# Optimization experiments

Hardware: AMD Instinct MI355X
Metric: run time of the kernel (lower is better)

The kernel has to match this reference:

```python
import jax, jax.numpy as jnp
import numpy as np

DIM = 192
N_HEADS = 8
HEAD_DIM = DIM // N_HEADS
SCALE = 1.0 / np.sqrt(HEAD_DIM).astype(np.float32)
H_GRID, W_GRID = 32, 64
KH, KW = 7, 11


def build_local_mask():
    # Equivalent to the torch double-loop construction: token (h2,w2) may attend
    # to (h,w) iff |h2-h| <= KH//2 and |w2-w| <= KW//2 (odd kernels).
    hh = jnp.arange(H_GRID)
    ww = jnp.arange(W_GRID)
    dh_ok = jnp.abs(hh[:, None] - hh[None, :]) <= KH // 2  # [H, H]
    dw_ok = jnp.abs(ww[:, None] - ww[None, :]) <= KW // 2  # [W, W]
    allowed = dh_ok[:, None, :, None] & dw_ok[None, :, None, :]  # [H, W, H, W]
    allowed = allowed.reshape(H_GRID * W_GRID, H_GRID * W_GRID)
    return jnp.where(allowed, 0.0, -jnp.inf).astype(jnp.float32)  # [N, N]


def setup_inputs() -> dict:
    key = jax.random.key(0)
    ks = jax.random.split(key, 5)
    B, N = 4, H_GRID * W_GRID
    w_std = 1.0 / np.sqrt(DIM)
    x = jax.random.normal(ks[0], (B, N, DIM), dtype=jnp.float32)
    qkv_w = jax.random.normal(ks[1], (3 * DIM, DIM), dtype=jnp.float32) * w_std
    qkv_b = jax.random.normal(ks[2], (3 * DIM,), dtype=jnp.float32) * 0.02
    proj_w = jax.random.normal(ks[3], (DIM, DIM), dtype=jnp.float32) * w_std
    proj_b = jax.random.normal(ks[4], (DIM,), dtype=jnp.float32) * 0.02
    mask = build_local_mask()
    return {"x": x, "qkv_w": qkv_w, "qkv_b": qkv_b,
            "proj_w": proj_w, "proj_b": proj_b, "mask": mask}


def reference(x, qkv_w, qkv_b, proj_w, proj_b, mask):
    B, N, _ = x.shape
    qkv = x @ qkv_w.T + qkv_b                              # [B, N, 3*DIM]
    qkv = qkv.reshape(B, N, 3, N_HEADS, HEAD_DIM)
    qkv = jnp.transpose(qkv, (2, 0, 3, 1, 4))              # [3, B, h, N, d]
    q, k, v = qkv[0] * SCALE, qkv[1], qkv[2]
    attn = jnp.einsum('bhnd,bhmd->bhnm', q, k) + mask      # [B, h, N, N]
    attn = jax.nn.softmax(attn, axis=-1)                   # == log_softmax().exp()
    out = jnp.einsum('bhnm,bhmd->bhnd', attn, v)           # [B, h, N, d]
    out = jnp.transpose(out, (0, 2, 1, 3)).reshape(B, N, DIM)
    return out @ proj_w.T + proj_b
```

## Files before the change

kernel.cpp:

```cpp
#include <hip/hip_runtime.h>
#include <math.h>

#define H_GRID 32
#define W_GRID 64
#define NTOK   2048
#define NHEADS 8
#define HD     24
#define DIMC   192
#define BATCH  4

static constexpr float SCALE = 0.20412414523193154f;

typedef unsigned short ushort;
typedef unsigned int   uint;
typedef __attribute__((ext_vector_type(8))) short bf16x8;
typedef __attribute__((ext_vector_type(4))) float f32x4;

static __device__ __forceinline__ float4 ld4(const float* p) { return *(const float4*)p; }

static __device__ __forceinline__ ushort f2bf(float f) {
    union { float f; uint u; } c; c.f = f;
    uint u = c.u;
    uint r = u + 0x7fffu + ((u >> 16) & 1u);
    return (ushort)(r >> 16);
}
static __device__ __forceinline__ float bf2f(ushort h) {
    union { uint u; float f; } c; c.u = ((uint)h) << 16; return c.f;
}

__global__ __launch_bounds__(256) void cast_w(const float* __restrict__ wq,
                                              const float* __restrict__ wp,
                                              ushort* __restrict__ wqhi, ushort* __restrict__ wqlo,
                                              ushort* __restrict__ wphi, ushort* __restrict__ wplo) {
    const int i = blockIdx.x * 256 + threadIdx.x;
    const float* src; ushort *dh, *dl; int off;
    if (i < 27648) { src = wq; dh = wqhi; dl = wqlo; off = i; }
    else           { src = wp; dh = wphi; dl = wplo; off = i - 27648; }
    float4 v = ld4(src + (size_t)off * 4);
    float a[4] = {v.x, v.y, v.z, v.w};
    ushort h[4], l[4];
#pragma unroll
    for (int j = 0; j < 4; j++) {
        h[j] = f2bf(a[j]);
        l[j] = f2bf(a[j] - bf2f(h[j]));
    }
    *(ushort4*)(dh + (size_t)off * 4) = make_ushort4(h[0], h[1], h[2], h[3]);
    *(ushort4*)(dl + (size_t)off * 4) = make_ushort4(l[0], l[1], l[2], l[3]);
}

__global__ __launch_bounds__(256) void gemm_qkv(const float* __restrict__ A,
                                                const ushort* __restrict__ Wh,
                                                const ushort* __restrict__ Wl,
                                                const float* __restrict__ bias,
                                                float* __restrict__ C) {
    __shared__ ushort Wsh[64 * 200];
    __shared__ ushort Wsl[64 * 200];

    const int t    = threadIdx.x;
    const int wave = t >> 6, lane = t & 63;
    const int m0   = blockIdx.x * 64 + wave * 16;
    const int j0   = blockIdx.y * 64;
    const int row  = lane & 15;
    const int kq   = lane >> 4;

    for (int i = t; i < 1536; i += 256) {
        const int r = i / 24, c = i - (i / 24) * 24;
        *(uint4*)&Wsh[r * 200 + c * 8] = *(const uint4*)&Wh[(size_t)(j0 + r) * 192 + c * 8];
        *(uint4*)&Wsl[r * 200 + c * 8] = *(const uint4*)&Wl[(size_t)(j0 + r) * 192 + c * 8];
    }

    const float* pA = A + (size_t)(m0 + row) * 192 + kq * 8;

    f32x4 acc[4] = {f32x4{0,0,0,0}, f32x4{0,0,0,0}, f32x4{0,0,0,0}, f32x4{0,0,0,0}};

    __syncthreads();

#pragma unroll
    for (int ks = 0; ks < 6; ks++) {
        float4 a0 = ld4(pA + ks * 32);
        float4 a1 = ld4(pA + ks * 32 + 4);
        float av[8] = {a0.x, a0.y, a0.z, a0.w, a1.x, a1.y, a1.z, a1.w};
        bf16x8 afh, afl;
#pragma unroll
        for (int j = 0; j < 8; j++) {
            ushort hh = f2bf(av[j]);
            afh[j] = (short)hh;
            afl[j] = (short)f2bf(av[j] - bf2f(hh));
        }
#pragma unroll
        for (int nt = 0; nt < 4; nt++) {
            const int widx = (nt * 16 + row) * 200 + kq * 8 + ks * 32;
            bf16x8 bh = *(const bf16x8*)&Wsh[widx];
            bf16x8 bl = *(const bf16x8*)&Wsl[widx];
            acc[nt] = __builtin_amdgcn_mfma_f32_16x16x32_bf16(afh, bh, acc[nt], 0, 0, 0);
            acc[nt] = __builtin_amdgcn_mfma_f32_16x16x32_bf16(afl, bh, acc[nt], 0, 0, 0);
            acc[nt] = __builtin_amdgcn_mfma_f32_16x16x32_bf16(afh, bl, acc[nt], 0, 0, 0);
        }
    }

#pragma unroll
    for (int nt = 0; nt < 4; nt++) {
        const int col = j0 + nt * 16 + row;
        const float bv = bias[col];
#pragma unroll
        for (int r = 0; r < 4; r++) {
            const int m = m0 + kq * 4 + r;
            C[(size_t)m * 576 + col] = acc[nt][r] + bv;
        }
    }
}

__global__ __launch_bounds__(256) void attn_mfma(const float* __restrict__ qkv,
                                                 ushort* __restrict__ ahi,
                                                 ushort* __restrict__ alo) {
    const int qtile = blockIdx.x;
    const int head  = blockIdx.y;
    const int b     = blockIdx.z;
    const int qh0   = (qtile >> 3) * 4;
    const int qw0   = (qtile & 7) * 8;

    const int kh0 = max(qh0 - 3, 0), kh1 = min(qh0 + 6, H_GRID - 1);
    const int kw0 = max(qw0 - 5, 0), kw1 = min(qw0 + 12, W_GRID - 1);
    const int khc = kh1 - kh0 + 1;
    const int kwc = kw1 - kw0 + 1;
    const int nk  = khc * kwc;

    const int t = threadIdx.x;
    const int w = t >> 6, lane = t & 63;
    const int n16 = lane & 15, quad = lane >> 4;

    __shared__ __align__(16) char sm[67584];
    ushort* Khi   = (ushort*)(sm);
    ushort* Klo   = (ushort*)(sm + 15360);
    ushort* Phi   = (ushort*)(sm);
    ushort* Plo   = (ushort*)(sm + 14848);
    ushort* Qhi   = (ushort*)(sm + 30720);
    ushort* Qlo   = (ushort*)(sm + 33280);
    ushort* VThi  = (ushort*)(sm + 35840);
    ushort* VTlo  = (ushort*)(sm + 50688);
    int*    khw   = (int*)(sm + 65536);
    int*    toks  = (int*)(sm + 66304);
    float*  mxbuf = (float*)(sm + 67072);
    float*  sumbuf= (float*)(sm + 67328);

    const float* base = qkv + (size_t)(b * 2048) * 576 + head * 24;

    if (t < 192) {
        if (t < nk) {
            const int rr = t / kwc;
            const int cc = t - rr * kwc;
            khw[t]  = ((kh0 + rr) << 8) | (kw0 + cc);
            toks[t] = ((kh0 + rr) << 6) + (kw0 + cc);
        } else {
            khw[t] = 0x7F7F;
        }
    }
    __syncthreads();

    for (int i = t; i < 768; i += 256) {
        const int s = i >> 2, g = i & 3;
        ushort h[8], l[8];
        if (g < 3 && s < nk) {
            const float* src = base + (size_t)toks[s] * 576 + 192 + g * 8;
            float4 a = ld4(src), c = ld4(src + 4);
            float vs[8] = {a.x, a.y, a.z, a.w, c.x, c.y, c.z, c.w};
#pragma unroll
            for (int j = 0; j < 8; j++) { h[j] = f2bf(vs[j]); l[j] = f2bf(vs[j] - bf2f(h[j])); }
        } else {
#pragma unroll
            for (int j = 0; j < 8; j++) { h[j] = 0; l[j] = 0; }
        }
        *(uint4*)&Khi[s * 40 + g * 8] = *(uint4*)h;
        *(uint4*)&Klo[s * 40 + g * 8] = *(uint4*)l;
    }
    if (t < 128) {
        const int r = t >> 2, g = t & 3;
        ushort h[8], l[8];
        if (g < 3) {
            const int tq = ((qh0 + (r >> 3)) << 6) + qw0 + (r & 7);
            const float* src = base + (size_t)tq * 576 + g * 8;
            float4 a = ld4(src), c = ld4(src + 4);
            float vs[8] = {a.x * SCALE, a.y * SCALE, a.z * SCALE, a.w * SCALE,
                           c.x * SCALE, c.y * SCALE, c.z * SCALE, c.w * SCALE};
#pragma unroll
            for (int j = 0; j < 8; j++) { h[j] = f2bf(vs[j]); l[j] = f2bf(vs[j] - bf2f(h[j])); }
        } else {
#pragma unroll
            for (int j = 0; j < 8; j++) { h[j] = 0; l[j] = 0; }
        }
        *(uint4*)&Qhi[r * 40 + g * 8] = *(uint4*)h;
        *(uint4*)&Qlo[r * 40 + g * 8] = *(uint4*)l;
    }
    for (int i = t; i < 1152; i += 256) {
        const int dq = i / 192, s = i - (i / 192) * 192;
        float4 vv = make_float4(0.f, 0.f, 0.f, 0.f);
        if (s < nk) vv = ld4(base + (size_t)toks[s] * 576 + 384 + dq * 4);
        float vs[4] = {vv.x, vv.y, vv.z, vv.w};
#pragma unroll
        for (int c = 0; c < 4; c++) {
            const int d = dq * 4 + c;
            ushort hh = f2bf(vs[c]);
            VThi[d * 232 + s] = hh;
            VTlo[d * 232 + s] = f2bf(vs[c] - bf2f(hh));
        }
    }
    for (int j = t; j < 1536; j += 256) {
        const int d = 24 + j / 192, s = j - (j / 192) * 192;
        VThi[d * 232 + s] = 0;
        VTlo[d * 232 + s] = 0;
    }
    __syncthreads();

    const int mt = w >> 1, nth = w & 1;
    const bf16x8 qfh = *(const bf16x8*)&Qhi[(16 * mt + n16) * 40 + quad * 8];
    const bf16x8 qfl = *(const bf16x8*)&Qlo[(16 * mt + n16) * 40 + quad * 8];

    f32x4 sc[6];
    int khwv[6];
#pragma unroll
    for (int j = 0; j < 6; j++) {
        const int slot = (nth * 6 + j) * 16 + n16;
        const bf16x8 kfh = *(const bf16x8*)&Khi[slot * 40 + quad * 8];
        const bf16x8 kfl = *(const bf16x8*)&Klo[slot * 40 + quad * 8];
        f32x4 a = f32x4{0, 0, 0, 0};
        a = __builtin_amdgcn_mfma_f32_16x16x32_bf16(qfh, kfh, a, 0, 0, 0);
        a = __builtin_amdgcn_mfma_f32_16x16x32_bf16(qfl, kfh, a, 0, 0, 0);
        a = __builtin_amdgcn_mfma_f32_16x16x32_bf16(qfh, kfl, a, 0, 0, 0);
        sc[j] = a;
        khwv[j] = khw[slot];
    }

    const int m0r = quad * 4;
    float sv[6][4];
    float mx4[4] = {-1e30f, -1e30f, -1e30f, -1e30f};
#pragma unroll
    for (int j = 0; j < 6; j++) {
        const int kh = khwv[j] >> 8, kw = khwv[j] & 255;
#pragma unroll
        for (int r = 0; r < 4; r++) {
            const int m = 16 * mt + m0r + r;
            const bool valid = (abs(kh - (qh0 + (m >> 3))) <= 3) &&
                               (abs(kw - (qw0 + (m & 7))) <= 5);
            const float s = valid ? sc[j][r] : -1e30f;
            sv[j][r] = s;
            mx4[r] = fmaxf(mx4[r], s);
        }
    }
#pragma unroll
    for (int d = 1; d < 16; d <<= 1)
#pragma unroll
        for (int r = 0; r < 4; r++) mx4[r] = fmaxf(mx4[r], __shfl_xor(mx4[r], d));
    if (n16 == 0) {
#pragma unroll
        for (int r = 0; r < 4; r++) mxbuf[w * 16 + m0r + r] = mx4[r];
    }
    __syncthreads();
#pragma unroll
    for (int r = 0; r < 4; r++) mx4[r] = fmaxf(mx4[r], mxbuf[(w ^ 1) * 16 + m0r + r]);

    float sum4[4] = {0.f, 0.f, 0.f, 0.f};
#pragma unroll
    for (int j = 0; j < 6; j++) {
        const int col = (nth * 6 + j) * 16 + n16;
#pragma unroll
        for (int r = 0; r < 4; r++) {
            const float p = __expf(sv[j][r] - mx4[r]);
            sum4[r] += p;
            const int m = 16 * mt + m0r + r;
            const ushort ph = f2bf(p);
            Phi[m * 232 + col] = ph;
            Plo[m * 232 + col] = f2bf(p - bf2f(ph));
        }
    }
#pragma unroll
    for (int d = 1; d < 16; d <<= 1)
#pragma unroll
        for (int r = 0; r < 4; r++) sum4[r] += __shfl_xor(sum4[r], d);
    if (n16 == 0) {
#pragma unroll
        for (int r = 0; r < 4; r++) sumbuf[w * 16 + m0r + r] = sum4[r];
    }
    __syncthreads();

    const int mtP = w >> 1, ntP = w & 1;
    f32x4 accA = f32x4{0,0,0,0}, accB = f32x4{0,0,0,0}, accC = f32x4{0,0,0,0};
#pragma unroll
    for (int ks = 0; ks < 6; ks++) {
        const int ko = ks * 32 + quad * 8;
        const bf16x8 pa = *(const bf16x8*)&Phi[(16 * mtP + n16) * 232 + ko];
        const bf16x8 pl = *(const bf16x8*)&Plo[(16 * mtP + n16) * 232 + ko];
        const bf16x8 va = *(const bf16x8*)&VThi[(16 * ntP + n16) * 232 + ko];
        const bf16x8 vl = *(const bf16x8*)&VTlo[(16 * ntP + n16) * 232 + ko];
        accA = __builtin_amdgcn_mfma_f32_16x16x32_bf16(pa, va, accA, 0, 0, 0);
        accB = __builtin_amdgcn_mfma_f32_16x16x32_bf16(pl, va, accB, 0, 0, 0);
        accC = __builtin_amdgcn_mfma_f32_16x16x32_bf16(pa, vl, accC, 0, 0, 0);
    }

    const int d = 16 * ntP + n16;
    if (d < 24) {
#pragma unroll
        for (int r = 0; r < 4; r++) {
            const int m   = 16 * mtP + quad * 4 + r;
            const float tot = sumbuf[(2 * mtP) * 16 + (m & 15)] +
                              sumbuf[(2 * mtP + 1) * 16 + (m & 15)];
            const float val = (accA[r] + accB[r] + accC[r]) / tot;
            const int tq = ((qh0 + (m >> 3)) << 6) + qw0 + (m & 7);
            const size_t ob = (size_t)(b * 2048 + tq) * 192 + head * 24 + d;
            const ushort hh = f2bf(val);
            ahi[ob] = hh;
            alo[ob] = f2bf(val - bf2f(hh));
        }
    }
}

__global__ __launch_bounds__(128) void gemm_proj(const ushort* __restrict__ Ahi,
                                                 const ushort* __restrict__ Alo,
                                                 const ushort* __restrict__ Wh,
                                                 const ushort* __restrict__ Wl,
                                                 const float* __restrict__ bias,
                                                 float* __restrict__ C) {
    __shared__ ushort Wsh[64 * 200];
    __shared__ ushort Wsl[64 * 200];

    const int t    = threadIdx.x;
    const int wave = t >> 6, lane = t & 63;
    const int m0   = blockIdx.x * 32 + wave * 16;
    const int j0   = blockIdx.y * 64;
    const int row  = lane & 15;
    const int kq   = lane >> 4;

    for (int i = t; i < 1536; i += 128) {
        const int r = i / 24, c = i - (i / 24) * 24;
        *(uint4*)&Wsh[r * 200 + c * 8] = *(const uint4*)&Wh[(size_t)(j0 + r) * 192 + c * 8];
        *(uint4*)&Wsl[r * 200 + c * 8] = *(const uint4*)&Wl[(size_t)(j0 + r) * 192 + c * 8];
    }

    const ushort* ah = Ahi + (size_t)(m0 + row) * 192 + kq * 8;
    const ushort* al = Alo + (size_t)(m0 + row) * 192 + kq * 8;

    f32x4 acc[4] = {f32x4{0,0,0,0}, f32x4{0,0,0,0}, f32x4{0,0,0,0}, f32x4{0,0,0,0}};

    __syncthreads();

#pragma unroll
    for (int ks = 0; ks < 6; ks++) {
        bf16x8 afh = *(const bf16x8*)(ah + ks * 32);
        bf16x8 afl = *(const bf16x8*)(al + ks * 32);
#pragma unroll
        for (int nt = 0; nt < 4; nt++) {
            const int widx = (nt * 16 + row) * 200 + kq * 8 + ks * 32;
            bf16x8 bh = *(const bf16x8*)&Wsh[widx];
            bf16x8 bl = *(const bf16x8*)&Wsl[widx];
            acc[nt] = __builtin_amdgcn_mfma_f32_16x16x32_bf16(afh, bh, acc[nt], 0, 0, 0);
            acc[nt] = __builtin_amdgcn_mfma_f32_16x16x32_bf16(afl, bh, acc[nt], 0, 0, 0);
            acc[nt] = __builtin_amdgcn_mfma_f32_16x16x32_bf16(afh, bl, acc[nt], 0, 0, 0);
        }
    }

#pragma unroll
    for (int nt = 0; nt < 4; nt++) {
        const int col = j0 + nt * 16 + row;
        const float bv = bias[col];
#pragma unroll
        for (int r = 0; r < 4; r++) {
            const int m = m0 + kq * 4 + r;
            C[(size_t)m * 192 + col] = acc[nt][r] + bv;
        }
    }
}

extern "C" void kernel_launch(void* const* d_in, const int* in_sizes, int n_in,
                              void* d_out, int out_size, void* d_ws, size_t ws_size,
                              hipStream_t stream) {
    const float* x      = (const float*)d_in[0];
    const float* qkv_w  = (const float*)d_in[1];
    const float* qkv_b  = (const float*)d_in[2];
    const float* proj_w = (const float*)d_in[3];
    const float* proj_b = (const float*)d_in[4];

    char* wsb = (char*)d_ws;
    float*  qkvws = (float*)(wsb + 0);
    ushort* awshi = (ushort*)(wsb + 18874368);
    ushort* awslo = (ushort*)(wsb + 22020096);
    ushort* wqhi  = (ushort*)(wsb + 25165824);
    ushort* wqlo  = (ushort*)(wsb + 25387008);
    ushort* wphi  = (ushort*)(wsb + 25608192);
    ushort* wplo  = (ushort*)(wsb + 25681920);
    float*  out   = (float*)d_out;

    hipLaunchKernelGGL(cast_w, dim3(144), dim3(256), 0, stream,
                       qkv_w, proj_w, wqhi, wqlo, wphi, wplo);
    hipLaunchKernelGGL(gemm_qkv, dim3(128, 9), dim3(256), 0, stream,
                       x, wqhi, wqlo, qkv_b, qkvws);
    hipLaunchKernelGGL(attn_mfma, dim3(64, 8, 4), dim3(256), 0, stream,
                       qkvws, awshi, awslo);
    hipLaunchKernelGGL(gemm_proj, dim3(256, 3), dim3(128), 0, stream,
                       awshi, awslo, wphi, wplo, proj_b, out);
}
```

Measured before the change: 134.9 us.

## Emit pre-split bf16 Q/K/V^T from QKV GEMM and read them directly in attention

The QKV GEMM epilogue now writes bf16 hi/lo pairs in per-head layouts: Q (pre-scaled) and K as [bh,token,32] and V transposed as [bh,d,token]. This lets the attention kernel load MFMA fragments straight from global memory instead of staging and converting K/Q/V through shared memory. The input x is also pre-split in the cast kernel, which zero-fills the pad columns. Attention now covers a fixed 10x32 key window with clamped addresses and masking, drops the P low-part term, and sums the rounded probabilities. This removes the fp32 qkv round trip and shared-memory staging, at the cost of more MFMA work on masked keys, uncoalesced global fragment reads, and slightly lower precision in P·V.

```diff
diff --git a/kernel.cpp b/kernel.cpp
--- a/kernel.cpp
+++ b/kernel.cpp
@@ -28,14 +28,29 @@
     union { uint u; float f; } c; c.u = ((uint)h) << 16; return c.f;
 }
 
-__global__ __launch_bounds__(256) void cast_w(const float* __restrict__ wq,
-                                              const float* __restrict__ wp,
-                                              ushort* __restrict__ wqhi, ushort* __restrict__ wqlo,
-                                              ushort* __restrict__ wphi, ushort* __restrict__ wplo) {
+__global__ __launch_bounds__(256) void cast_split(const float* __restrict__ x,
+                                                  const float* __restrict__ wq,
+                                                  const float* __restrict__ wp,
+                                                  ushort* __restrict__ xhi, ushort* __restrict__ xlo,
+                                                  ushort* __restrict__ wqhi, ushort* __restrict__ wqlo,
+                                                  ushort* __restrict__ wphi, ushort* __restrict__ wplo,
+                                                  ushort* __restrict__ Qhi, ushort* __restrict__ Qlo,
+                                                  ushort* __restrict__ Khi, ushort* __restrict__ Klo) {
     const int i = blockIdx.x * 256 + threadIdx.x;
+    if (i >= 430080) {
+        const int ti = i - 430080;
+        const int tensor = ti >> 16;
+        const int row = ti & 65535;
+        ushort* dst = (tensor == 0) ? Qhi : (tensor == 1) ? Qlo
+                    : (tensor == 2) ? Khi : Klo;
+        const uint4 z = {0u, 0u, 0u, 0u};
+        *(uint4*)&dst[(size_t)row * 32 + 24] = z;
+        return;
+    }
     const float* src; ushort *dh, *dl; int off;
-    if (i < 27648) { src = wq; dh = wqhi; dl = wqlo; off = i; }
-    else           { src = wp; dh = wphi; dl = wplo; off = i - 27648; }
+    if (i < 393216)      { src = x;  dh = xhi;  dl = xlo;  off = i; }
+    else if (i < 420864) { src = wq; dh = wqhi; dl = wqlo; off = i - 393216; }
+    else                 { src = wp; dh = wphi; dl = wplo; off = i - 420864; }
     float4 v = ld4(src + (size_t)off * 4);
     float a[4] = {v.x, v.y, v.z, v.w};
     ushort h[4], l[4];
@@ -48,11 +63,14 @@
     *(ushort4*)(dl + (size_t)off * 4) = make_ushort4(l[0], l[1], l[2], l[3]);
 }
 
-__global__ __launch_bounds__(256) void gemm_qkv(const float* __restrict__ A,
+__global__ __launch_bounds__(256) void gemm_qkv(const ushort* __restrict__ Ahi,
+                                                const ushort* __restrict__ Alo,
                                                 const ushort* __restrict__ Wh,
                                                 const ushort* __restrict__ Wl,
                                                 const float* __restrict__ bias,
-                                                float* __restrict__ C) {
+                                                ushort* __restrict__ Qhi, ushort* __restrict__ Qlo,
+                                                ushort* __restrict__ Khi, ushort* __restrict__ Klo,
+                                                ushort* __restrict__ VThi, ushort* __restrict__ VTlo) {
     __shared__ ushort Wsh[64 * 200];
     __shared__ ushort Wsl[64 * 200];
 
@@ -69,7 +87,8 @@
         *(uint4*)&Wsl[r * 200 + c * 8] = *(const uint4*)&Wl[(size_t)(j0 + r) * 192 + c * 8];
     }
 
-    const float* pA = A + (size_t)(m0 + row) * 192 + kq * 8;
+    const ushort* ah = Ahi + (size_t)(m0 + row) * 192 + kq * 8;
+    const ushort* al = Alo + (size_t)(m0 + row) * 192 + kq * 8;
 
     f32x4 acc[4] = {f32x4{0,0,0,0}, f32x4{0,0,0,0}, f32x4{0,0,0,0}, f32x4{0,0,0,0}};
 
@@ -77,16 +96,8 @@
 
 #pragma unroll
     for (int ks = 0; ks < 6; ks++) {
-        float4 a0 = ld4(pA + ks * 32);
-        float4 a1 = ld4(pA + ks * 32 + 4);
-        float av[8] = {a0.x, a0.y, a0.z, a0.w, a1.x, a1.y, a1.z, a1.w};
-        bf16x8 afh, afl;
-#pragma unroll
-        for (int j = 0; j < 8; j++) {
-            ushort hh = f2bf(av[j]);
-            afh[j] = (short)hh;
-            afl[j] = (short)f2bf(av[j] - bf2f(hh));
-        }
+        bf16x8 afh = *(const bf16x8*)(ah + ks * 32);
+        bf16x8 afl = *(const bf16x8*)(al + ks * 32);
 #pragma unroll
         for (int nt = 0; nt < 4; nt++) {
             const int widx = (nt * 16 + row) * 200 + kq * 8 + ks * 32;
@@ -98,19 +109,49 @@
         }
     }
 
+    const int band = blockIdx.y / 3;
+    const int tok0 = (m0 + kq * 4) & 2047;
+    const int b_   = (m0 + kq * 4) >> 11;
 #pragma unroll
     for (int nt = 0; nt < 4; nt++) {
         const int col = j0 + nt * 16 + row;
+        const int lc  = col - band * 192;
+        const int h_  = lc / 24;
+        const int d_  = lc - h_ * 24;
         const float bv = bias[col];
-#pragma unroll
-        for (int r = 0; r < 4; r++) {
-            const int m = m0 + kq * 4 + r;
-            C[(size_t)m * 576 + col] = acc[nt][r] + bv;
-        }
-    }
-}
-
-__global__ __launch_bounds__(256) void attn_mfma(const float* __restrict__ qkv,
+        if (band == 2) {
+            ushort vh[4], vl[4];
+#pragma unroll
+            for (int r = 0; r < 4; r++) {
+                const float val = acc[nt][r] + bv;
+                vh[r] = f2bf(val);
+                vl[r] = f2bf(val - bf2f(vh[r]));
+            }
+            const size_t addr = ((size_t)(b_ * 8 + h_) * 32 + d_) * 2048 + tok0;
+            *(ushort4*)&VThi[addr] = make_ushort4(vh[0], vh[1], vh[2], vh[3]);
+            *(ushort4*)&VTlo[addr] = make_ushort4(vl[0], vl[1], vl[2], vl[3]);
+        } else {
+            ushort* dh = band ? Khi : Qhi;
+            ushort* dl = band ? Klo : Qlo;
+            const float sc_ = band ? 1.0f : SCALE;
+#pragma unroll
+            for (int r = 0; r < 4; r++) {
+                const float val = (acc[nt][r] + bv) * sc_;
+                const ushort hh = f2bf(val);
+                const size_t addr = ((size_t)(b_ * 8 + h_) * 2048 + tok0 + r) * 32 + d_;
+                dh[addr] = hh;
+                dl[addr] = f2bf(val - bf2f(hh));
+            }
+        }
+    }
+}
+
+__global__ __launch_bounds__(256) void attn_mfma(const ushort* __restrict__ Qhi,
+                                                 const ushort* __restrict__ Qlo,
+                                                 const ushort* __restrict__ Khi,
+                                                 const ushort* __restrict__ Klo,
+                                                 const ushort* __restrict__ VThi,
+                                                 const ushort* __restrict__ VTlo,
                                                  ushort* __restrict__ ahi,
                                                  ushort* __restrict__ alo) {
     const int qtile = blockIdx.x;
@@ -118,130 +159,56 @@
     const int b     = blockIdx.z;
     const int qh0   = (qtile >> 3) * 4;
     const int qw0   = (qtile & 7) * 8;
-
-    const int kh0 = max(qh0 - 3, 0), kh1 = min(qh0 + 6, H_GRID - 1);
-    const int kw0 = max(qw0 - 5, 0), kw1 = min(qw0 + 12, W_GRID - 1);
-    const int khc = kh1 - kh0 + 1;
-    const int kwc = kw1 - kw0 + 1;
-    const int nk  = khc * kwc;
+    const int kw0a  = max(qw0 - 8, 0);
 
     const int t = threadIdx.x;
     const int w = t >> 6, lane = t & 63;
     const int n16 = lane & 15, quad = lane >> 4;
-
-    __shared__ __align__(16) char sm[67584];
-    ushort* Khi   = (ushort*)(sm);
-    ushort* Klo   = (ushort*)(sm + 15360);
-    ushort* Phi   = (ushort*)(sm);
-    ushort* Plo   = (ushort*)(sm + 14848);
-    ushort* Qhi   = (ushort*)(sm + 30720);
-    ushort* Qlo   = (ushort*)(sm + 33280);
-    ushort* VThi  = (ushort*)(sm + 35840);
-    ushort* VTlo  = (ushort*)(sm + 50688);
-    int*    khw   = (int*)(sm + 65536);
-    int*    toks  = (int*)(sm + 66304);
-    float*  mxbuf = (float*)(sm + 67072);
-    float*  sumbuf= (float*)(sm + 67328);
-
-    const float* base = qkv + (size_t)(b * 2048) * 576 + head * 24;
-
-    if (t < 192) {
-        if (t < nk) {
-            const int rr = t / kwc;
-            const int cc = t - rr * kwc;
-            khw[t]  = ((kh0 + rr) << 8) | (kw0 + cc);
-            toks[t] = ((kh0 + rr) << 6) + (kw0 + cc);
-        } else {
-            khw[t] = 0x7F7F;
-        }
-    }
-    __syncthreads();
-
-    for (int i = t; i < 768; i += 256) {
-        const int s = i >> 2, g = i & 3;
-        ushort h[8], l[8];
-        if (g < 3 && s < nk) {
-            const float* src = base + (size_t)toks[s] * 576 + 192 + g * 8;
-            float4 a = ld4(src), c = ld4(src + 4);
-            float vs[8] = {a.x, a.y, a.z, a.w, c.x, c.y, c.z, c.w};
-#pragma unroll
-            for (int j = 0; j < 8; j++) { h[j] = f2bf(vs[j]); l[j] = f2bf(vs[j] - bf2f(h[j])); }
-        } else {
-#pragma unroll
-            for (int j = 0; j < 8; j++) { h[j] = 0; l[j] = 0; }
-        }
-        *(uint4*)&Khi[s * 40 + g * 8] = *(uint4*)h;
-        *(uint4*)&Klo[s * 40 + g * 8] = *(uint4*)l;
-    }
-    if (t < 128) {
-        const int r = t >> 2, g = t & 3;
-        ushort h[8], l[8];
-        if (g < 3) {
-            const int tq = ((qh0 + (r >> 3)) << 6) + qw0 + (r & 7);
-            const float* src = base + (size_t)tq * 576 + g * 8;
-            float4 a = ld4(src), c = ld4(src + 4);
-            float vs[8] = {a.x * SCALE, a.y * SCALE, a.z * SCALE, a.w * SCALE,
-                           c.x * SCALE, c.y * SCALE, c.z * SCALE, c.w * SCALE};
-#pragma unroll
-            for (int j = 0; j < 8; j++) { h[j] = f2bf(vs[j]); l[j] = f2bf(vs[j] - bf2f(h[j])); }
-        } else {
-#pragma unroll
-            for (int j = 0; j < 8; j++) { h[j] = 0; l[j] = 0; }
-        }
-        *(uint4*)&Qhi[r * 40 + g * 8] = *(uint4*)h;
-        *(uint4*)&Qlo[r * 40 + g * 8] = *(uint4*)l;
-    }
-    for (int i = t; i < 1152; i += 256) {
-        const int dq = i / 192, s = i - (i / 192) * 192;
-        float4 vv = make_float4(0.f, 0.f, 0.f, 0.f);
-        if (s < nk) vv = ld4(base + (size_t)toks[s] * 576 + 384 + dq * 4);
-        float vs[4] = {vv.x, vv.y, vv.z, vv.w};
-#pragma unroll
-        for (int c = 0; c < 4; c++) {
-            const int d = dq * 4 + c;
-            ushort hh = f2bf(vs[c]);
-            VThi[d * 232 + s] = hh;
-            VTlo[d * 232 + s] = f2bf(vs[c] - bf2f(hh));
-        }
-    }
-    for (int j = t; j < 1536; j += 256) {
-        const int d = 24 + j / 192, s = j - (j / 192) * 192;
-        VThi[d * 232 + s] = 0;
-        VTlo[d * 232 + s] = 0;
-    }
-    __syncthreads();
+    const int bh = b * 8 + head;
+
+    __shared__ ushort Phi[32 * 328];
+    __shared__ float  mxbuf[64];
+    __shared__ float  sumbuf[64];
+
+    const ushort* Qh_b = Qhi + (size_t)bh * 2048 * 32;
+    const ushort* Ql_b = Qlo + (size_t)bh * 2048 * 32;
+    const ushort* Kh_b = Khi + (size_t)bh * 2048 * 32;
+    const ushort* Kl_b = Klo + (size_t)bh * 2048 * 32;
+    const ushort* Vh_b = VThi + (size_t)bh * 32 * 2048;
+    const ushort* Vl_b = VTlo + (size_t)bh * 32 * 2048;
 
     const int mt = w >> 1, nth = w & 1;
-    const bf16x8 qfh = *(const bf16x8*)&Qhi[(16 * mt + n16) * 40 + quad * 8];
-    const bf16x8 qfl = *(const bf16x8*)&Qlo[(16 * mt + n16) * 40 + quad * 8];
-
-    f32x4 sc[6];
-    int khwv[6];
-#pragma unroll
-    for (int j = 0; j < 6; j++) {
-        const int slot = (nth * 6 + j) * 16 + n16;
-        const bf16x8 kfh = *(const bf16x8*)&Khi[slot * 40 + quad * 8];
-        const bf16x8 kfl = *(const bf16x8*)&Klo[slot * 40 + quad * 8];
+
+    const int mrow = 16 * mt + n16;
+    const int tq_a = ((qh0 + (mrow >> 3)) << 6) + qw0 + (mrow & 7);
+    const bf16x8 qfh = *(const bf16x8*)&Qh_b[(size_t)tq_a * 32 + quad * 8];
+    const bf16x8 qfl = *(const bf16x8*)&Ql_b[(size_t)tq_a * 32 + quad * 8];
+
+    const int m0r = quad * 4;
+    float sv[10][4];
+    float mx4[4] = {-3e38f, -3e38f, -3e38f, -3e38f};
+#pragma unroll
+    for (int j = 0; j < 10; j++) {
+        const int slot = (nth * 10 + j) * 16 + n16;
+        const int rr = slot >> 5, cc = slot & 31;
+        const int khv = qh0 - 3 + rr;
+        const int kwv = kw0a + cc;
+        const int kh_cl = min(max(khv, 0), 31);
+        const int tok   = (kh_cl << 6) + min(kwv, 63);
+        const bf16x8 kfh = *(const bf16x8*)&Kh_b[(size_t)tok * 32 + quad * 8];
+        const bf16x8 kfl = *(const bf16x8*)&Kl_b[(size_t)tok * 32 + quad * 8];
         f32x4 a = f32x4{0, 0, 0, 0};
         a = __builtin_amdgcn_mfma_f32_16x16x32_bf16(qfh, kfh, a, 0, 0, 0);
         a = __builtin_amdgcn_mfma_f32_16x16x32_bf16(qfl, kfh, a, 0, 0, 0);
         a = __builtin_amdgcn_mfma_f32_16x16x32_bf16(qfh, kfl, a, 0, 0, 0);
-        sc[j] = a;
-        khwv[j] = khw[slot];
-    }
-
-    const int m0r = quad * 4;
-    float sv[6][4];
-    float mx4[4] = {-1e30f, -1e30f, -1e30f, -1e30f};
-#pragma unroll
-    for (int j = 0; j < 6; j++) {
-        const int kh = khwv[j] >> 8, kw = khwv[j] & 255;
+        const bool khok = (khv >= 0) && (khv < 32) && (kwv < 64);
 #pragma unroll
         for (int r = 0; r < 4; r++) {
-            const int m = 16 * mt + m0r + r;
-            const bool valid = (abs(kh - (qh0 + (m >> 3))) <= 3) &&
-                               (abs(kw - (qw0 + (m & 7))) <= 5);
-            const float s = valid ? sc[j][r] : -1e30f;
+            const int m   = 16 * mt + m0r + r;
+            const int qhv = qh0 + (m >> 3);
+            const int qwv = qw0 + (m & 7);
+            const bool valid = khok && (abs(khv - qhv) <= 3) && (abs(kwv - qwv) <= 5);
+            const float s = valid ? a[r] : -3e38f;
             sv[j][r] = s;
             mx4[r] = fmaxf(mx4[r], s);
         }
@@ -260,16 +227,14 @@
 
     float sum4[4] = {0.f, 0.f, 0.f, 0.f};
 #pragma unroll
-    for (int j = 0; j < 6; j++) {
-        const int col = (nth * 6 + j) * 16 + n16;
+    for (int j = 0; j < 10; j++) {
+        const int col = (nth * 10 + j) * 16 + n16;
 #pragma unroll
         for (int r = 0; r < 4; r++) {
             const float p = __expf(sv[j][r] - mx4[r]);
-            sum4[r] += p;
-            const int m = 16 * mt + m0r + r;
             const ushort ph = f2bf(p);
-            Phi[m * 232 + col] = ph;
-            Plo[m * 232 + col] = f2bf(p - bf2f(ph));
+            sum4[r] += bf2f(ph);
+            Phi[(16 * mt + m0r + r) * 328 + col] = ph;
         }
     }
 #pragma unroll
@@ -283,29 +248,29 @@
     __syncthreads();
 
     const int mtP = w >> 1, ntP = w & 1;
-    f32x4 accA = f32x4{0,0,0,0}, accB = f32x4{0,0,0,0}, accC = f32x4{0,0,0,0};
-#pragma unroll
-    for (int ks = 0; ks < 6; ks++) {
-        const int ko = ks * 32 + quad * 8;
-        const bf16x8 pa = *(const bf16x8*)&Phi[(16 * mtP + n16) * 232 + ko];
-        const bf16x8 pl = *(const bf16x8*)&Plo[(16 * mtP + n16) * 232 + ko];
-        const bf16x8 va = *(const bf16x8*)&VThi[(16 * ntP + n16) * 232 + ko];
-        const bf16x8 vl = *(const bf16x8*)&VTlo[(16 * ntP + n16) * 232 + ko];
-        accA = __builtin_amdgcn_mfma_f32_16x16x32_bf16(pa, va, accA, 0, 0, 0);
-        accB = __builtin_amdgcn_mfma_f32_16x16x32_bf16(pl, va, accB, 0, 0, 0);
-        accC = __builtin_amdgcn_mfma_f32_16x16x32_bf16(pa, vl, accC, 0, 0, 0);
-    }
-
-    const int d = 16 * ntP + n16;
-    if (d < 24) {
+    const int dr  = 16 * ntP + n16;
+    f32x4 accA = f32x4{0,0,0,0}, accB = f32x4{0,0,0,0};
+#pragma unroll
+    for (int ks = 0; ks < 10; ks++) {
+        const int khv   = qh0 - 3 + ks;
+        const int kh_cl = min(max(khv, 0), 31);
+        const int seg   = min((kh_cl << 6) + kw0a + quad * 8, 2040);
+        const bf16x8 pa = *(const bf16x8*)&Phi[(16 * mtP + n16) * 328 + ks * 32 + quad * 8];
+        const bf16x8 vh = *(const bf16x8*)&Vh_b[(size_t)dr * 2048 + seg];
+        const bf16x8 vl = *(const bf16x8*)&Vl_b[(size_t)dr * 2048 + seg];
+        accA = __builtin_amdgcn_mfma_f32_16x16x32_bf16(pa, vh, accA, 0, 0, 0);
+        accB = __builtin_amdgcn_mfma_f32_16x16x32_bf16(pa, vl, accB, 0, 0, 0);
+    }
+
+    if (dr < 24) {
 #pragma unroll
         for (int r = 0; r < 4; r++) {
-            const int m   = 16 * mtP + quad * 4 + r;
+            const int m = 16 * mtP + quad * 4 + r;
             const float tot = sumbuf[(2 * mtP) * 16 + (m & 15)] +
                               sumbuf[(2 * mtP + 1) * 16 + (m & 15)];
-            const float val = (accA[r] + accB[r] + accC[r]) / tot;
+            const float val = (accA[r] + accB[r]) / tot;
             const int tq = ((qh0 + (m >> 3)) << 6) + qw0 + (m & 7);
-            const size_t ob = (size_t)(b * 2048 + tq) * 192 + head * 24 + d;
+            const size_t ob = (size_t)(b * 2048 + tq) * 192 + head * 24 + dr;
             const ushort hh = f2bf(val);
             ahi[ob] = hh;
             alo[ob] = f2bf(val - bf2f(hh));
@@ -379,21 +344,30 @@
     const float* proj_b = (const float*)d_in[4];
 
     char* wsb = (char*)d_ws;
-    float*  qkvws = (float*)(wsb + 0);
-    ushort* awshi = (ushort*)(wsb + 18874368);
-    ushort* awslo = (ushort*)(wsb + 22020096);
-    ushort* wqhi  = (ushort*)(wsb + 25165824);
-    ushort* wqlo  = (ushort*)(wsb + 25387008);
-    ushort* wphi  = (ushort*)(wsb + 25608192);
-    ushort* wplo  = (ushort*)(wsb + 25681920);
+    ushort* xhi   = (ushort*)(wsb + 0);
+    ushort* xlo   = (ushort*)(wsb + 3145728);
+    ushort* wqhi  = (ushort*)(wsb + 6291456);
+    ushort* wqlo  = (ushort*)(wsb + 6512640);
+    ushort* wphi  = (ushort*)(wsb + 6733824);
+    ushort* wplo  = (ushort*)(wsb + 6807552);
+    ushort* awshi = (ushort*)(wsb + 6881280);
+    ushort* awslo = (ushort*)(wsb + 10027008);
+    ushort* Qhi   = (ushort*)(wsb + 13172736);
+    ushort* Qlo   = (ushort*)(wsb + 17367040);
+    ushort* Khi   = (ushort*)(wsb + 21561344);
+    ushort* Klo   = (ushort*)(wsb + 25755648);
+    ushort* VThi  = (ushort*)(wsb + 29949952);
+    ushort* VTlo  = (ushort*)(wsb + 34144256);
     float*  out   = (float*)d_out;
 
-    hipLaunchKernelGGL(cast_w, dim3(144), dim3(256), 0, stream,
-                       qkv_w, proj_w, wqhi, wqlo, wphi, wplo);
+    hipLaunchKernelGGL(cast_split, dim3(2704), dim3(256), 0, stream,
+                       x, qkv_w, proj_w, xhi, xlo, wqhi, wqlo, wphi, wplo,
+                       Qhi, Qlo, Khi, Klo);
     hipLaunchKernelGGL(gemm_qkv, dim3(128, 9), dim3(256), 0, stream,
-                       x, wqhi, wqlo, qkv_b, qkvws);
+                       xhi, xlo, wqhi, wqlo, qkv_b,
+                       Qhi, Qlo, Khi, Klo, VThi, VTlo);
     hipLaunchKernelGGL(attn_mfma, dim3(64, 8, 4), dim3(256), 0, stream,
-                       qkvws, awshi, awslo);
+                       Qhi, Qlo, Khi, Klo, VThi, VTlo, awshi, awslo);
     hipLaunchKernelGGL(gemm_proj, dim3(256, 3), dim3(128), 0, stream,
                        awshi, awslo, wphi, wplo, proj_b, out);
 }
```

After: 142.6 us. +5.7%, slower.
